# Optimization experiments

Hardware: AMD Instinct MI355X
Metric: run time of the kernel (lower is better)

## Reference

```python
import jax, jax.numpy as jnp
import numpy as np

EPS_LN = 1e-5


def segment_softmax(logits, seg, num_segments):
    m = jax.ops.segment_max(logits, seg, num_segments=num_segments)
    e = jnp.exp(logits - m[seg])
    s = jax.ops.segment_sum(e, seg, num_segments=num_segments)
    return e / (s[seg] + 1e-16)


def transformer_conv(x, src, dst, edge_attr, Wq, bq, Wk, bk, Wv, bv, We, Ws, bs):
    # PyG TransformerConv, heads=1: key/value gathered at source, query at dst,
    # transformed edge feature added to both key and value (message).
    N, D = x.shape[0], Wq.shape[1]
    q = (x @ Wq + bq)[dst]                      # [E, D]
    e = edge_attr @ We                          # [E, D] (lin_edge, no bias)
    k = (x @ Wk + bk)[src] + e                  # [E, D]
    v = (x @ Wv + bv)[src] + e                  # [E, D]
    alpha = segment_softmax((q * k).sum(-1) / jnp.sqrt(jnp.float32(D)), dst, N)
    agg = jax.ops.segment_sum(alpha[:, None] * v, dst, num_segments=N)
    return agg + x @ Ws + bs                    # root_weight skip connection


def graph_layer_norm(x, w, b):
    # PyG LayerNorm mode='graph': normalize over all nodes AND features of the graph.
    mu = x.mean()
    xc = x - mu
    var = (xc * xc).mean()
    return xc * jax.lax.rsqrt(var + EPS_LN) * w + b


def setup_inputs():
    key = jax.random.key(0)
    ks = jax.random.split(key, 32)
    N, E, F_NODE, F_EDGE, H, D_OUT = 50000, 800000, 64, 16, 128, 1
    g = lambda k, shp, s=0.05: jax.random.normal(k, shp, jnp.float32) * s
    inp = {
        'x': jax.random.normal(ks[0], (N, F_NODE), jnp.float32),
        'edge_index': jax.random.randint(ks[1], (2, E), 0, N),
        'edge_attr': jax.random.normal(ks[2], (E, F_EDGE), jnp.float32),
        'fc1_w': g(ks[3], (F_NODE, H)), 'fc1_b': jnp.zeros((H,), jnp.float32),
        'c1_Wq': g(ks[4], (H, H)), 'c1_bq': jnp.zeros((H,), jnp.float32),
        'c1_Wk': g(ks[5], (H, H)), 'c1_bk': jnp.zeros((H,), jnp.float32),
        'c1_Wv': g(ks[6], (H, H)), 'c1_bv': jnp.zeros((H,), jnp.float32),
        'c1_We': g(ks[7], (F_EDGE, H)),
        'c1_Ws': g(ks[8], (H, H)), 'c1_bs': jnp.zeros((H,), jnp.float32),
        'ln1_w': jnp.ones((H,), jnp.float32), 'ln1_b': jnp.zeros((H,), jnp.float32),
        'c2_Wq': g(ks[9], (H, H)), 'c2_bq': jnp.zeros((H,), jnp.float32),
        'c2_Wk': g(ks[10], (H, H)), 'c2_bk': jnp.zeros((H,), jnp.float32),
        'c2_Wv': g(ks[11], (H, H)), 'c2_bv': jnp.zeros((H,), jnp.float32),
        'c2_We': g(ks[12], (F_EDGE, H)),
        'c2_Ws': g(ks[13], (H, H)), 'c2_bs': jnp.zeros((H,), jnp.float32),
        'ln2_w': jnp.ones((H,), jnp.float32), 'ln2_b': jnp.zeros((H,), jnp.float32),
        'fc2_w': g(ks[14], (H, D_OUT)), 'fc2_b': jnp.zeros((D_OUT,), jnp.float32),
    }
    return inp


def reference(x, edge_index, edge_attr,
              fc1_w, fc1_b,
              c1_Wq, c1_bq, c1_Wk, c1_bk, c1_Wv, c1_bv, c1_We, c1_Ws, c1_bs,
              ln1_w, ln1_b,
              c2_Wq, c2_bq, c2_Wk, c2_bk, c2_Wv, c2_bv, c2_We, c2_Ws, c2_bs,
              ln2_w, ln2_b,
              fc2_w, fc2_b):
    src, dst = edge_index[0], edge_index[1]
    hx = x @ fc1_w + fc1_b
    h = transformer_conv(hx, src, dst, edge_attr,
                         c1_Wq, c1_bq, c1_Wk, c1_bk, c1_Wv, c1_bv, c1_We, c1_Ws, c1_bs)
    h = jax.nn.relu(graph_layer_norm(h, ln1_w, ln1_b))
    h = transformer_conv(h, src, dst, edge_attr,
                         c2_Wq, c2_bq, c2_Wk, c2_bk, c2_Wv, c2_bv, c2_We, c2_Ws, c2_bs)
    h = jax.nn.relu(graph_layer_norm(h, ln2_w, ln2_b))
    return h @ fc2_w + fc2_b
```

## Files before the change

### kernel.cpp

```cpp
#include <hip/hip_runtime.h>
#include <math.h>

#define HH 128
#define FIN 64
#define FE 16
#define SCAN_CHUNK 512

__global__ __launch_bounds__(256) void zero_int4(int4* __restrict__ p, int n4) {
  const int stride = gridDim.x * 256;
  for (int i = blockIdx.x * 256 + threadIdx.x; i < n4; i += stride)
    p[i] = make_int4(0, 0, 0, 0);
}

__global__ __launch_bounds__(256) void hist_kernel(
    const int* __restrict__ dstArr, int* __restrict__ deg, int E) {
  const int e = blockIdx.x * 256 + threadIdx.x;
  if (e < E) atomicAdd(deg + dstArr[e], 1);
}

__global__ __launch_bounds__(256) void scan1(
    const int* __restrict__ deg, int* __restrict__ out, int* __restrict__ sums, int n) {
  __shared__ int lds[256];
  const int t = threadIdx.x;
  const int i0 = blockIdx.x * SCAN_CHUNK + t * 2;
  const int v0 = (i0 < n) ? deg[i0] : 0;
  const int v1 = (i0 + 1 < n) ? deg[i0 + 1] : 0;
  const int tsum = v0 + v1;
  lds[t] = tsum;
  __syncthreads();
  for (int off = 1; off < 256; off <<= 1) {
    const int x = (t >= off) ? lds[t - off] : 0;
    __syncthreads();
    lds[t] += x;
    __syncthreads();
  }
  const int excl = lds[t] - tsum;
  if (i0 < n) out[i0] = excl;
  if (i0 + 1 < n) out[i0 + 1] = excl + v0;
  if (t == 255) sums[blockIdx.x] = lds[255];
}

__global__ __launch_bounds__(256) void scan2(int* __restrict__ sums, int nb) {
  __shared__ int lds[256];
  const int t = threadIdx.x;
  const int v = (t < nb) ? sums[t] : 0;
  lds[t] = v;
  __syncthreads();
  for (int off = 1; off < 256; off <<= 1) {
    const int x = (t >= off) ? lds[t - off] : 0;
    __syncthreads();
    lds[t] += x;
    __syncthreads();
  }
  if (t < nb) sums[t] = lds[t] - v;
}

__global__ __launch_bounds__(256) void scan3(
    int* __restrict__ out, const int* __restrict__ sums, int n) {
  const int add = sums[blockIdx.x];
  const int i0 = blockIdx.x * SCAN_CHUNK + threadIdx.x * 2;
  if (i0 < n) out[i0] += add;
  if (i0 + 1 < n) out[i0 + 1] += add;
}

__global__ __launch_bounds__(256) void scatter_kernel(
    const int* __restrict__ dstArr, const int* __restrict__ off,
    int* __restrict__ cursor, int* __restrict__ eids, int E) {
  const int e = blockIdx.x * 256 + threadIdx.x;
  if (e < E) {
    const int d = dstArr[e];
    const int p = atomicAdd(cursor + d, 1);
    eids[off[d] + p] = e;
  }
}

template<int K, int RB>
__global__ __launch_bounds__(128) void gemm_rows(
    const float* __restrict__ in, const float* __restrict__ W,
    const float* __restrict__ bias, float* __restrict__ out, int nrows) {
  __shared__ float tile[RB * K];
  const int r0 = blockIdx.x * RB;
  const int tid = threadIdx.x;
  {
    const int rows = min(RB, nrows - r0);
    const int cnt = rows * K / 4;
    const float4* src = (const float4*)(in + (size_t)r0 * K);
    float4* dst = (float4*)tile;
    for (int i = tid; i < cnt; i += 128) dst[i] = src[i];
  }
  __syncthreads();
  const int j = tid;
  float acc[RB];
  const float bj = bias[j];
#pragma unroll
  for (int r = 0; r < RB; ++r) acc[r] = bj;
#pragma unroll 4
  for (int k = 0; k < K; ++k) {
    float w = W[k * HH + j];
#pragma unroll
    for (int r = 0; r < RB; ++r) acc[r] += tile[r * K + k] * w;
  }
#pragma unroll
  for (int r = 0; r < RB; ++r) {
    int row = r0 + r;
    if (row < nrows) out[(size_t)row * HH + j] = acc[r];
  }
}

template<int RB>
__global__ __launch_bounds__(128) void qkvs_kernel(
    float* __restrict__ x,
    const float* __restrict__ Wq, const float* __restrict__ bq,
    const float* __restrict__ Wk, const float* __restrict__ bk,
    const float* __restrict__ Wv, const float* __restrict__ bv,
    const float* __restrict__ Ws, const float* __restrict__ bs,
    float* __restrict__ q, float* __restrict__ k, float* __restrict__ v,
    int nrows) {
  __shared__ float tile[RB * HH];
  const int r0 = blockIdx.x * RB;
  const int tid = threadIdx.x;
  {
    const int rows = min(RB, nrows - r0);
    const int cnt = rows * HH / 4;
    const float4* src = (const float4*)(x + (size_t)r0 * HH);
    float4* dst = (float4*)tile;
    for (int i = tid; i < cnt; i += 128) dst[i] = src[i];
  }
  __syncthreads();
  const int j = tid;
  float aq[RB], ak[RB], av[RB], as_[RB];
  const float bqj = bq[j], bkj = bk[j], bvj = bv[j], bsj = bs[j];
#pragma unroll
  for (int r = 0; r < RB; ++r) { aq[r] = bqj; ak[r] = bkj; av[r] = bvj; as_[r] = bsj; }
#pragma unroll 2
  for (int kk = 0; kk < HH; ++kk) {
    const float wq = Wq[kk * HH + j];
    const float wk = Wk[kk * HH + j];
    const float wv = Wv[kk * HH + j];
    const float ws = Ws[kk * HH + j];
#pragma unroll
    for (int r = 0; r < RB; ++r) {
      const float xv = tile[r * HH + kk];
      aq[r] += xv * wq; ak[r] += xv * wk; av[r] += xv * wv; as_[r] += xv * ws;
    }
  }
#pragma unroll
  for (int r = 0; r < RB; ++r) {
    int row = r0 + r;
    if (row < nrows) {
      const size_t o = (size_t)row * HH + j;
      q[o] = aq[r]; k[o] = ak[r]; v[o] = av[r]; x[o] = as_[r];
    }
  }
}

__global__ __launch_bounds__(128) void qe_kernel(
    const float* __restrict__ q, const float* __restrict__ We,
    float* __restrict__ qe, int N) {
  __shared__ float qs[8 * HH];
  __shared__ float WeT[HH * 17];
  const int tid = threadIdx.x;
  for (int u = tid; u < FE * HH; u += 128) {
    const int i = u >> 7, j = u & 127;
    WeT[j * 17 + i] = We[u];
  }
  const int r0 = blockIdx.x * 8;
  const int rows = min(8, N - r0);
  const int cnt4 = rows * (HH / 4);
  const float4* src = (const float4*)(q + (size_t)r0 * HH);
  for (int u = tid; u < cnt4; u += 128) ((float4*)qs)[u] = src[u];
  __syncthreads();
  const int r = tid >> 4, i = tid & 15;
  if (r < rows) {
    const float* qrow = qs + r * HH;
    float acc = 0.f;
#pragma unroll 8
    for (int j = 0; j < HH; ++j) acc += qrow[j] * WeT[j * 17 + i];
    qe[(size_t)(r0 + r) * FE + i] = acc;
  }
}

__global__ __launch_bounds__(256) void dst_conv16(
    const int* __restrict__ csr_off, const int* __restrict__ deg,
    const int* __restrict__ csr_eid, const int* __restrict__ srcArr,
    const float* __restrict__ ea, const float* __restrict__ We,
    const float* __restrict__ q, const float* __restrict__ qe,
    const float* __restrict__ k, const float* __restrict__ v,
    float* __restrict__ xio, double* __restrict__ partials, int N) {
  __shared__ float WeS[FE * HH];
  for (int u = threadIdx.x; u < FE * HH; u += 256) WeS[u] = We[u];
  __syncthreads();
  const int lane = threadIdx.x & 63;
  const int gl = lane & 15;
  const int gbase = lane & 48;
  const int grp = (blockIdx.x * 256 + threadIdx.x) >> 4;
  const int ngrp = (gridDim.x * 256) >> 4;
  const float rs = 0.088388347648318447f;
  float s = 0.f, sq = 0.f;
  for (int d = grp; d < N; d += ngrp) {
    const int off = csr_off[d];
    const int cnt = deg[d];
    const float4* qp = (const float4*)(q + (size_t)d * HH);
    const float4 qc0 = qp[gl], qc1 = qp[16 + gl];
    const float qel = qe[(size_t)d * FE + gl];
    float4 a0 = {0.f, 0.f, 0.f, 0.f}, a1 = {0.f, 0.f, 0.f, 0.f};
    float wsum = 0.f, t = 0.f;
    int eid = (cnt > 0) ? csr_eid[off] : 0;
    int sn = (cnt > 0) ? srcArr[eid] : 0;
    for (int i = 0; i < cnt; ++i) {
      const bool nxt = (i + 1 < cnt);
      const int eid_n = nxt ? csr_eid[off + i + 1] : 0;
      const int sn_n = nxt ? srcArr[eid_n] : 0;
      const float eal = ea[(size_t)eid * FE + gl];
      const float4* kp = (const float4*)(k + (size_t)sn * HH);
      const float4* vp = (const float4*)(v + (size_t)sn * HH);
      const float4 kc0 = kp[gl], kc1 = kp[16 + gl];
      const float4 vc0 = vp[gl], vc1 = vp[16 + gl];
      float part = qc0.x * kc0.x + qc0.y * kc0.y + qc0.z * kc0.z + qc0.w * kc0.w
                 + qc1.x * kc1.x + qc1.y * kc1.y + qc1.z * kc1.z + qc1.w * kc1.w
                 + qel * eal;
      part += __shfl_xor(part, 1);
      part += __shfl_xor(part, 2);
      part += __shfl_xor(part, 4);
      part += __shfl_xor(part, 8);
      const float w = __expf(part * rs);
      wsum += w;
      a0.x += w * vc0.x; a0.y += w * vc0.y; a0.z += w * vc0.z; a0.w += w * vc0.w;
      a1.x += w * vc1.x; a1.y += w * vc1.y; a1.z += w * vc1.z; a1.w += w * vc1.w;
      t += w * eal;
      eid = eid_n;
      sn = sn_n;
    }
    float4 c0 = {0.f, 0.f, 0.f, 0.f}, c1 = {0.f, 0.f, 0.f, 0.f};
#pragma unroll
    for (int i = 0; i < FE; ++i) {
      const float ti = __shfl(t, gbase + i);
      const float4 w0 = *(const float4*)(WeS + i * HH + gl * 4);
      const float4 w1 = *(const float4*)(WeS + i * HH + 64 + gl * 4);
      c0.x += ti * w0.x; c0.y += ti * w0.y; c0.z += ti * w0.z; c0.w += ti * w0.w;
      c1.x += ti * w1.x; c1.y += ti * w1.y; c1.z += ti * w1.z; c1.w += ti * w1.w;
    }
    const float inv = 1.0f / (wsum + 1e-16f);
    float4* xr = (float4*)(xio + (size_t)d * HH);
    const float4 sk0 = xr[gl], sk1 = xr[16 + gl];
    float4 o0, o1;
    o0.x = fmaf(a0.x + c0.x, inv, sk0.x);
    o0.y = fmaf(a0.y + c0.y, inv, sk0.y);
    o0.z = fmaf(a0.z + c0.z, inv, sk0.z);
    o0.w = fmaf(a0.w + c0.w, inv, sk0.w);
    o1.x = fmaf(a1.x + c1.x, inv, sk1.x);
    o1.y = fmaf(a1.y + c1.y, inv, sk1.y);
    o1.z = fmaf(a1.z + c1.z, inv, sk1.z);
    o1.w = fmaf(a1.w + c1.w, inv, sk1.w);
    xr[gl] = o0;
    xr[16 + gl] = o1;
    s += o0.x + o0.y + o0.z + o0.w + o1.x + o1.y + o1.z + o1.w;
    sq += o0.x * o0.x + o0.y * o0.y + o0.z * o0.z + o0.w * o0.w
        + o1.x * o1.x + o1.y * o1.y + o1.z * o1.z + o1.w * o1.w;
  }
#pragma unroll
  for (int o = 32; o; o >>= 1) {
    s += __shfl_xor(s, o);
    sq += __shfl_xor(sq, o);
  }
  __shared__ double red[8];
  const int w = threadIdx.x >> 6;
  if ((threadIdx.x & 63) == 0) { red[w * 2] = (double)s; red[w * 2 + 1] = (double)sq; }
  __syncthreads();
  if (threadIdx.x == 0) {
    partials[(size_t)blockIdx.x * 2] = red[0] + red[2] + red[4] + red[6];
    partials[(size_t)blockIdx.x * 2 + 1] = red[1] + red[3] + red[5] + red[7];
  }
}

__global__ __launch_bounds__(256) void ln_reduce2(
    const double* __restrict__ partials, int nb, float* __restrict__ stats,
    double inv_count) {
  double s = 0.0, sq = 0.0;
  for (int i = threadIdx.x; i < nb; i += 256) {
    s += partials[(size_t)i * 2];
    sq += partials[(size_t)i * 2 + 1];
  }
#pragma unroll
  for (int off = 32; off; off >>= 1) {
    s += __shfl_xor(s, off);
    sq += __shfl_xor(sq, off);
  }
  __shared__ double red[8];
  const int w = threadIdx.x >> 6;
  if ((threadIdx.x & 63) == 0) { red[w * 2] = s; red[w * 2 + 1] = sq; }
  __syncthreads();
  if (threadIdx.x == 0) {
    double S = 0, SQ = 0;
    for (int i = 0; i < 4; ++i) { S += red[i * 2]; SQ += red[i * 2 + 1]; }
    const double mu = S * inv_count;
    const double var = SQ * inv_count - mu * mu;
    stats[0] = (float)mu;
    stats[1] = (float)(1.0 / sqrt(var + 1e-5));
  }
}

__global__ __launch_bounds__(256) void ln_apply(
    float* __restrict__ x, const float* __restrict__ stats,
    const float* __restrict__ w, const float* __restrict__ b, int total4) {
  const int i = blockIdx.x * 256 + threadIdx.x;
  if (i >= total4) return;
  const float mu = stats[0], rstd = stats[1];
  const float4 xv = ((const float4*)x)[i];
  const float4 wv = ((const float4*)w)[i & 31];
  const float4 bv = ((const float4*)b)[i & 31];
  float4 o;
  o.x = fmaxf(fmaf((xv.x - mu) * rstd, wv.x, bv.x), 0.f);
  o.y = fmaxf(fmaf((xv.y - mu) * rstd, wv.y, bv.y), 0.f);
  o.z = fmaxf(fmaf((xv.z - mu) * rstd, wv.z, bv.z), 0.f);
  o.w = fmaxf(fmaf((xv.w - mu) * rstd, wv.w, bv.w), 0.f);
  ((float4*)x)[i] = o;
}

__global__ __launch_bounds__(256) void fc2_kernel(
    const float* __restrict__ h, const float* __restrict__ w,
    const float* __restrict__ b, float* __restrict__ out, int n) {
  const int lane = threadIdx.x & 63;
  const int node = (blockIdx.x * blockDim.x + threadIdx.x) >> 6;
  if (node >= n) return;
  const float2 hv = *(const float2*)(h + (size_t)node * HH + lane * 2);
  const float2 wv = *(const float2*)(w + lane * 2);
  float p = hv.x * wv.x + hv.y * wv.y;
#pragma unroll
  for (int off = 32; off; off >>= 1) p += __shfl_xor(p, off);
  if (lane == 0) out[node] = p + b[0];
}

extern "C" void kernel_launch(void* const* d_in, const int* in_sizes, int n_in,
                              void* d_out, int out_size, void* d_ws, size_t ws_size,
                              hipStream_t stream) {
  const float* x      = (const float*)d_in[0];
  const int*   eidx   = (const int*)d_in[1];
  const float* ea     = (const float*)d_in[2];
  const float* fc1_w  = (const float*)d_in[3];
  const float* fc1_b  = (const float*)d_in[4];
  const float* c1_Wq  = (const float*)d_in[5];
  const float* c1_bq  = (const float*)d_in[6];
  const float* c1_Wk  = (const float*)d_in[7];
  const float* c1_bk  = (const float*)d_in[8];
  const float* c1_Wv  = (const float*)d_in[9];
  const float* c1_bv  = (const float*)d_in[10];
  const float* c1_We  = (const float*)d_in[11];
  const float* c1_Ws  = (const float*)d_in[12];
  const float* c1_bs  = (const float*)d_in[13];
  const float* ln1_w  = (const float*)d_in[14];
  const float* ln1_b  = (const float*)d_in[15];
  const float* c2_Wq  = (const float*)d_in[16];
  const float* c2_bq  = (const float*)d_in[17];
  const float* c2_Wk  = (const float*)d_in[18];
  const float* c2_bk  = (const float*)d_in[19];
  const float* c2_Wv  = (const float*)d_in[20];
  const float* c2_bv  = (const float*)d_in[21];
  const float* c2_We  = (const float*)d_in[22];
  const float* c2_Ws  = (const float*)d_in[23];
  const float* c2_bs  = (const float*)d_in[24];
  const float* ln2_w  = (const float*)d_in[25];
  const float* ln2_b  = (const float*)d_in[26];
  const float* fc2_w  = (const float*)d_in[27];
  const float* fc2_b  = (const float*)d_in[28];

  const int N = in_sizes[0] / FIN;
  const int E = in_sizes[2] / FE;
  const int* srcA = eidx;
  const int* dstA = eidx + E;

  float* ws    = (float*)d_ws;
  const size_t NH = (size_t)N * HH;
  float* bufX  = ws;
  float* qb    = ws + NH;
  float* kb    = ws + 2 * NH;
  float* vb    = ws + 3 * NH;
  int* ibase   = (int*)(ws + 4 * NH);
  int* deg     = ibase;
  int* cursor  = ibase + N;
  int* csr_off = ibase + 2 * N;
  int* csr_eid = ibase + 3 * N;
  size_t icnt  = ((size_t)3 * N + E + 3) & ~(size_t)3;
  float* qeb   = (float*)(ibase + icnt);
  double* partials = (double*)(qeb + (size_t)N * FE);
  const int NB = 2048;
  float* stats = (float*)(partials + 2 * NB);
  int* sums    = (int*)(stats + 4);

  const int total4 = (int)(NH / 4);
  const int gRows  = (N + 15) / 16;
  const int gE     = (E + 255) / 256;
  const int nb1    = (N + SCAN_CHUNK - 1) / SCAN_CHUNK;
  const int gQe    = (N + 7) / 8;
  const double invC = 1.0 / (double)NH;

  zero_int4<<<128, 256, 0, stream>>>((int4*)deg, (2 * N + 3) / 4);
  hist_kernel<<<gE, 256, 0, stream>>>(dstA, deg, E);
  scan1<<<nb1, 256, 0, stream>>>(deg, csr_off, sums, N);
  scan2<<<1, 256, 0, stream>>>(sums, nb1);
  scan3<<<nb1, 256, 0, stream>>>(csr_off, sums, N);
  scatter_kernel<<<gE, 256, 0, stream>>>(dstA, csr_off, cursor, csr_eid, E);

  gemm_rows<FIN, 16><<<gRows, 128, 0, stream>>>(x, fc1_w, fc1_b, bufX, N);
  qkvs_kernel<16><<<gRows, 128, 0, stream>>>(bufX, c1_Wq, c1_bq, c1_Wk, c1_bk,
                                             c1_Wv, c1_bv, c1_Ws, c1_bs,
                                             qb, kb, vb, N);
  qe_kernel<<<gQe, 128, 0, stream>>>(qb, c1_We, qeb, N);
  dst_conv16<<<NB, 256, 0, stream>>>(csr_off, deg, csr_eid, srcA, ea, c1_We,
                                     qb, qeb, kb, vb, bufX, partials, N);
  ln_reduce2<<<1, 256, 0, stream>>>(partials, NB, stats, invC);
  ln_apply<<<(total4 + 255) / 256, 256, 0, stream>>>(bufX, stats, ln1_w, ln1_b, total4);

  qkvs_kernel<16><<<gRows, 128, 0, stream>>>(bufX, c2_Wq, c2_bq, c2_Wk, c2_bk,
                                             c2_Wv, c2_bv, c2_Ws, c2_bs,
                                             qb, kb, vb, N);
  qe_kernel<<<gQe, 128, 0, stream>>>(qb, c2_We, qeb, N);
  dst_conv16<<<NB, 256, 0, stream>>>(csr_off, deg, csr_eid, srcA, ea, c2_We,
                                     qb, qeb, kb, vb, bufX, partials, N);
  ln_reduce2<<<1, 256, 0, stream>>>(partials, NB, stats, invC);
  ln_apply<<<(total4 + 255) / 256, 256, 0, stream>>>(bufX, stats, ln2_w, ln2_b, total4);

  fc2_kernel<<<(N + 3) / 4, 256, 0, stream>>>(bufX, fc2_w, fc2_b, (float*)d_out, N);
}
```

Measured before the change: 937.0 us.

## Interleave K/V rows, unroll edge loop by four, one node group per thread-group

Stores K and V for each node in one interleaved 256-float row, so each gathered source node's key and value sit contiguously. The per-destination edge loop is unrolled by four, putting more independent gathers in flight. The grid-stride loop is replaced by one 16-lane group per node, with the block count and partials array sized from N. This targets gather latency in the attention aggregation, at the cost of higher register pressure and a larger partials reduction.

```diff
diff --git a/kernel.cpp b/kernel.cpp
--- a/kernel.cpp
+++ b/kernel.cpp
@@ -114,7 +114,7 @@
     const float* __restrict__ Wk, const float* __restrict__ bk,
     const float* __restrict__ Wv, const float* __restrict__ bv,
     const float* __restrict__ Ws, const float* __restrict__ bs,
-    float* __restrict__ q, float* __restrict__ k, float* __restrict__ v,
+    float* __restrict__ q, float* __restrict__ kv,
     int nrows) {
   __shared__ float tile[RB * HH];
   const int r0 = blockIdx.x * RB;
@@ -149,7 +149,11 @@
     int row = r0 + r;
     if (row < nrows) {
       const size_t o = (size_t)row * HH + j;
-      q[o] = aq[r]; k[o] = ak[r]; v[o] = av[r]; x[o] = as_[r];
+      const size_t ko = (size_t)row * 256 + j;
+      q[o] = aq[r];
+      kv[ko] = ak[r];
+      kv[ko + HH] = av[r];
+      x[o] = as_[r];
     }
   }
 }
@@ -185,7 +189,7 @@
     const int* __restrict__ csr_eid, const int* __restrict__ srcArr,
     const float* __restrict__ ea, const float* __restrict__ We,
     const float* __restrict__ q, const float* __restrict__ qe,
-    const float* __restrict__ k, const float* __restrict__ v,
+    const float* __restrict__ kv,
     float* __restrict__ xio, double* __restrict__ partials, int N) {
   __shared__ float WeS[FE * HH];
   for (int u = threadIdx.x; u < FE * HH; u += 256) WeS[u] = We[u];
@@ -193,11 +197,10 @@
   const int lane = threadIdx.x & 63;
   const int gl = lane & 15;
   const int gbase = lane & 48;
-  const int grp = (blockIdx.x * 256 + threadIdx.x) >> 4;
-  const int ngrp = (gridDim.x * 256) >> 4;
+  const int d = (blockIdx.x * 256 + threadIdx.x) >> 4;
   const float rs = 0.088388347648318447f;
   float s = 0.f, sq = 0.f;
-  for (int d = grp; d < N; d += ngrp) {
+  if (d < N) {
     const int off = csr_off[d];
     const int cnt = deg[d];
     const float4* qp = (const float4*)(q + (size_t)d * HH);
@@ -205,38 +208,87 @@
     const float qel = qe[(size_t)d * FE + gl];
     float4 a0 = {0.f, 0.f, 0.f, 0.f}, a1 = {0.f, 0.f, 0.f, 0.f};
     float wsum = 0.f, t = 0.f;
-    int eid = (cnt > 0) ? csr_eid[off] : 0;
-    int sn = (cnt > 0) ? srcArr[eid] : 0;
-    for (int i = 0; i < cnt; ++i) {
-      const bool nxt = (i + 1 < cnt);
-      const int eid_n = nxt ? csr_eid[off + i + 1] : 0;
-      const int sn_n = nxt ? srcArr[eid_n] : 0;
-      const float eal = ea[(size_t)eid * FE + gl];
-      const float4* kp = (const float4*)(k + (size_t)sn * HH);
-      const float4* vp = (const float4*)(v + (size_t)sn * HH);
-      const float4 kc0 = kp[gl], kc1 = kp[16 + gl];
-      const float4 vc0 = vp[gl], vc1 = vp[16 + gl];
-      float part = qc0.x * kc0.x + qc0.y * kc0.y + qc0.z * kc0.z + qc0.w * kc0.w
-                 + qc1.x * kc1.x + qc1.y * kc1.y + qc1.z * kc1.z + qc1.w * kc1.w
-                 + qel * eal;
-      part += __shfl_xor(part, 1);
-      part += __shfl_xor(part, 2);
-      part += __shfl_xor(part, 4);
-      part += __shfl_xor(part, 8);
-      const float w = __expf(part * rs);
-      wsum += w;
-      a0.x += w * vc0.x; a0.y += w * vc0.y; a0.z += w * vc0.z; a0.w += w * vc0.w;
-      a1.x += w * vc1.x; a1.y += w * vc1.y; a1.z += w * vc1.z; a1.w += w * vc1.w;
-      t += w * eal;
-      eid = eid_n;
-      sn = sn_n;
+    int i = 0;
+    for (; i + 4 <= cnt; i += 4) {
+      const int b = off + i;
+      const int e0 = csr_eid[b], e1 = csr_eid[b + 1];
+      const int e2 = csr_eid[b + 2], e3 = csr_eid[b + 3];
+      const int s0 = srcArr[e0], s1 = srcArr[e1];
+      const int s2 = srcArr[e2], s3 = srcArr[e3];
+      const float A0 = ea[(size_t)e0 * FE + gl];
+      const float A1 = ea[(size_t)e1 * FE + gl];
+      const float A2 = ea[(size_t)e2 * FE + gl];
+      const float A3 = ea[(size_t)e3 * FE + gl];
+      const float4* K0 = (const float4*)(kv + (size_t)s0 * 256);
+      const float4* K1 = (const float4*)(kv + (size_t)s1 * 256);
+      const float4* K2 = (const float4*)(kv + (size_t)s2 * 256);
+      const float4* K3 = (const float4*)(kv + (size_t)s3 * 256);
+      const float4 k00 = K0[gl], k01 = K0[16 + gl];
+      const float4 k10 = K1[gl], k11 = K1[16 + gl];
+      const float4 k20 = K2[gl], k21 = K2[16 + gl];
+      const float4 k30 = K3[gl], k31 = K3[16 + gl];
+      const float4 v00 = K0[32 + gl], v01 = K0[48 + gl];
+      const float4 v10 = K1[32 + gl], v11 = K1[48 + gl];
+      const float4 v20 = K2[32 + gl], v21 = K2[48 + gl];
+      const float4 v30 = K3[32 + gl], v31 = K3[48 + gl];
+      float p0 = qc0.x * k00.x + qc0.y * k00.y + qc0.z * k00.z + qc0.w * k00.w
+               + qc1.x * k01.x + qc1.y * k01.y + qc1.z * k01.z + qc1.w * k01.w
+               + qel * A0;
+      float p1 = qc0.x * k10.x + qc0.y * k10.y + qc0.z * k10.z + qc0.w * k10.w
+               + qc1.x * k11.x + qc1.y * k11.y + qc1.z * k11.z + qc1.w * k11.w
+               + qel * A1;
+      float p2 = qc0.x * k20.x + qc0.y * k20.y + qc0.z * k20.z + qc0.w * k20.w
+               + qc1.x * k21.x + qc1.y * k21.y + qc1.z * k21.z + qc1.w * k21.w
+               + qel * A2;
+      float p3 = qc0.x * k30.x + qc0.y * k30.y + qc0.z * k30.z + qc0.w * k30.w
+               + qc1.x * k31.x + qc1.y * k31.y + qc1.z * k31.z + qc1.w * k31.w
+               + qel * A3;
+#pragma unroll
+      for (int m = 1; m < 16; m <<= 1) {
+        p0 += __shfl_xor(p0, m);
+        p1 += __shfl_xor(p1, m);
+        p2 += __shfl_xor(p2, m);
+        p3 += __shfl_xor(p3, m);
+      }
+      const float w0 = __expf(p0 * rs);
+      const float w1 = __expf(p1 * rs);
+      const float w2 = __expf(p2 * rs);
+      const float w3 = __expf(p3 * rs);
+      a0.x += w0 * v00.x + w1 * v10.x + w2 * v20.x + w3 * v30.x;
+      a0.y += w0 * v00.y + w1 * v10.y + w2 * v20.y + w3 * v30.y;
+      a0.z += w0 * v00.z + w1 * v10.z + w2 * v20.z + w3 * v30.z;
+      a0.w += w0 * v00.w + w1 * v10.w + w2 * v20.w + w3 * v30.w;
+      a1.x += w0 * v01.x + w1 * v11.x + w2 * v21.x + w3 * v31.x;
+      a1.y += w0 * v01.y + w1 * v11.y + w2 * v21.y + w3 * v31.y;
+      a1.z += w0 * v01.z + w1 * v11.z + w2 * v21.z + w3 * v31.z;
+      a1.w += w0 * v01.w + w1 * v11.w + w2 * v21.w + w3 * v31.w;
+      wsum += (w0 + w1) + (w2 + w3);
+      t += w0 * A0 + w1 * A1 + w2 * A2 + w3 * A3;
+    }
+    for (; i < cnt; ++i) {
+      const int e0 = csr_eid[off + i];
+      const int s0 = srcArr[e0];
+      const float A0 = ea[(size_t)e0 * FE + gl];
+      const float4* K0 = (const float4*)(kv + (size_t)s0 * 256);
+      const float4 k00 = K0[gl], k01 = K0[16 + gl];
+      const float4 v00 = K0[32 + gl], v01 = K0[48 + gl];
+      float p0 = qc0.x * k00.x + qc0.y * k00.y + qc0.z * k00.z + qc0.w * k00.w
+               + qc1.x * k01.x + qc1.y * k01.y + qc1.z * k01.z + qc1.w * k01.w
+               + qel * A0;
+#pragma unroll
+      for (int m = 1; m < 16; m <<= 1) p0 += __shfl_xor(p0, m);
+      const float w0 = __expf(p0 * rs);
+      wsum += w0;
+      a0.x += w0 * v00.x; a0.y += w0 * v00.y; a0.z += w0 * v00.z; a0.w += w0 * v00.w;
+      a1.x += w0 * v01.x; a1.y += w0 * v01.y; a1.z += w0 * v01.z; a1.w += w0 * v01.w;
+      t += w0 * A0;
     }
     float4 c0 = {0.f, 0.f, 0.f, 0.f}, c1 = {0.f, 0.f, 0.f, 0.f};
 #pragma unroll
-    for (int i = 0; i < FE; ++i) {
-      const float ti = __shfl(t, gbase + i);
-      const float4 w0 = *(const float4*)(WeS + i * HH + gl * 4);
-      const float4 w1 = *(const float4*)(WeS + i * HH + 64 + gl * 4);
+    for (int ii = 0; ii < FE; ++ii) {
+      const float ti = __shfl(t, gbase + ii);
+      const float4 w0 = *(const float4*)(WeS + ii * HH + gl * 4);
+      const float4 w1 = *(const float4*)(WeS + ii * HH + 64 + gl * 4);
       c0.x += ti * w0.x; c0.y += ti * w0.y; c0.z += ti * w0.z; c0.w += ti * w0.w;
       c1.x += ti * w1.x; c1.y += ti * w1.y; c1.z += ti * w1.z; c1.w += ti * w1.w;
     }
@@ -373,8 +425,7 @@
   const size_t NH = (size_t)N * HH;
   float* bufX  = ws;
   float* qb    = ws + NH;
-  float* kb    = ws + 2 * NH;
-  float* vb    = ws + 3 * NH;
+  float* kvb   = ws + 2 * NH;
   int* ibase   = (int*)(ws + 4 * NH);
   int* deg     = ibase;
   int* cursor  = ibase + N;
@@ -383,7 +434,7 @@
   size_t icnt  = ((size_t)3 * N + E + 3) & ~(size_t)3;
   float* qeb   = (float*)(ibase + icnt);
   double* partials = (double*)(qeb + (size_t)N * FE);
-  const int NB = 2048;
+  const int NB = (N * 16 + 255) / 256;
   float* stats = (float*)(partials + 2 * NB);
   int* sums    = (int*)(stats + 4);
 
@@ -404,19 +455,19 @@
   gemm_rows<FIN, 16><<<gRows, 128, 0, stream>>>(x, fc1_w, fc1_b, bufX, N);
   qkvs_kernel<16><<<gRows, 128, 0, stream>>>(bufX, c1_Wq, c1_bq, c1_Wk, c1_bk,
                                              c1_Wv, c1_bv, c1_Ws, c1_bs,
-                                             qb, kb, vb, N);
+                                             qb, kvb, N);
   qe_kernel<<<gQe, 128, 0, stream>>>(qb, c1_We, qeb, N);
   dst_conv16<<<NB, 256, 0, stream>>>(csr_off, deg, csr_eid, srcA, ea, c1_We,
-                                     qb, qeb, kb, vb, bufX, partials, N);
+                                     qb, qeb, kvb, bufX, partials, N);
   ln_reduce2<<<1, 256, 0, stream>>>(partials, NB, stats, invC);
   ln_apply<<<(total4 + 255) / 256, 256, 0, stream>>>(bufX, stats, ln1_w, ln1_b, total4);
 
   qkvs_kernel<16><<<gRows, 128, 0, stream>>>(bufX, c2_Wq, c2_bq, c2_Wk, c2_bk,
                                              c2_Wv, c2_bv, c2_Ws, c2_bs,
-                                             qb, kb, vb, N);
+                                             qb, kvb, N);
   qe_kernel<<<gQe, 128, 0, stream>>>(qb, c2_We, qeb, N);
   dst_conv16<<<NB, 256, 0, stream>>>(csr_off, deg, csr_eid, srcA, ea, c2_We,
-                                     qb, qeb, kb, vb, bufX, partials, N);
+                                     qb, qeb, kvb, bufX, partials, N);
   ln_reduce2<<<1, 256, 0, stream>>>(partials, NB, stats, invC);
   ln_apply<<<(total4 + 255) / 256, 256, 0, stream>>>(bufX, stats, ln2_w, ln2_b, total4);
 
```

Result: faster. 813.7 us (-13.2%).
